# Kernel optimization log

Measured on AMD Instinct MI355X. Metric: run time of the kernel, lower is better.

The kernel has to match this reference:

```python
import jax, jax.numpy as jnp
import numpy as np

N = 100000      # nodes
E = 1600000     # edges (avg degree 16)
F_IN, F_HID, F_OUT = 128, 64, 47


def setup_inputs() -> dict:
    key = jax.random.key(0)
    k1, k2, k3, k4 = jax.random.split(key, 4)
    x = jax.random.normal(k1, (N, F_IN), jnp.float32)
    edge_index = jax.random.randint(k2, (2, E), 0, N, jnp.int32)
    W1 = jax.random.normal(k3, (F_IN, F_HID), jnp.float32) * (1.0 / np.sqrt(F_IN))
    b1 = jnp.zeros((F_HID,), jnp.float32)
    W2 = jax.random.normal(k4, (F_HID, F_OUT), jnp.float32) * (1.0 / np.sqrt(F_HID))
    b2 = jnp.zeros((F_OUT,), jnp.float32)
    return {"x": x, "edge_index": edge_index, "W1": W1, "b1": b1, "W2": W2, "b2": b2}


def _gcn_conv(x, W, b, src, dst, n):
    """GCNConv with self-loops and symmetric normalization:
       out = D^{-1/2} (A + I) D^{-1/2} X W + b
    """
    xw = x @ W                                   # [N, F_out] transform first (small GEMM)
    # degree of A + I computed over destination nodes
    deg = jnp.ones((n,), xw.dtype).at[dst].add(1.0)      # [N]
    dinv = jax.lax.rsqrt(deg)                            # deg^{-1/2}
    norm = dinv[src] * dinv[dst]                         # [E]
    msg = xw[src] * norm[:, None]                        # [E, F_out] gather
    agg = jnp.zeros_like(xw).at[dst].add(msg)            # scatter-add aggregate
    agg = agg + xw * (1.0 / deg)[:, None]                # self-loop term: norm = 1/deg
    return agg + b


def reference(x, edge_index, W1, b1, W2, b2):
    src, dst = edge_index[0], edge_index[1]
    n = x.shape[0]
    h = _gcn_conv(x, W1, b1, src, dst, n)
    h = jax.nn.relu(h)
    # dropout is identity in eval mode (deterministic baseline)
    h = _gcn_conv(h, W2, b2, src, dst, n)
    return jax.nn.log_softmax(h, axis=1)
```

## Files before the change

### kernel.cpp

```cpp
#include <hip/hip_runtime.h>
#include <hip/hip_bf16.h>
#include <math.h>


#define CAP 48
#define NBSHIFT 8
#define SCNODES 256
#define BCAP 6144
typedef unsigned short u16;

__device__ __forceinline__ u16 f2bf(float f) {
    __hip_bfloat16 h = __float2bfloat16(f);
    return *reinterpret_cast<u16*>(&h);
}
__device__ __forceinline__ float bf2f(u16 u) {
    return __uint_as_float(((unsigned)u) << 16);
}


#define KC 32
#define KCP 36
#define FUSED_SMEM 18944

__global__ __launch_bounds__(256) void gemm1_bin(const float* __restrict__ X,
                                                 const float* __restrict__ W,
                                                 u16* __restrict__ OUT,
                                                 const int* __restrict__ src,
                                                 const int* __restrict__ dst,
                                                 int* __restrict__ gtail,
                                                 int* __restrict__ bucketed,
                                                 int N, int E, int NB, int seg, int BINB) {
    __shared__ __align__(16) char smem[FUSED_SMEM];
    const int t = threadIdx.x;

    if ((int)blockIdx.x >= BINB) {
        float* xs = (float*)smem;
        float* Wp = (float*)(smem + 64 * KCP * 4);
        const int row0 = (blockIdx.x - BINB) * 64;
        const int c4 = (t & 15) * 4;
        const int r4 = (t >> 4) * 4;
        float acc[4][4] = {};

        for (int k0 = 0; k0 < 128; k0 += KC) {
            const float4* W4 = reinterpret_cast<const float4*>(W + k0 * 64);
            #pragma unroll
            for (int i = t; i < KC * 16; i += 256)
                reinterpret_cast<float4*>(Wp)[i] = W4[i];
            #pragma unroll
            for (int i = t; i < 64 * 8; i += 256) {
                int r = i >> 3, kq = i & 7;
                int m = row0 + r;
                float4 v = make_float4(0.f, 0.f, 0.f, 0.f);
                if (m < N) v = *reinterpret_cast<const float4*>(&X[(size_t)m * 128 + k0 + kq * 4]);
                *reinterpret_cast<float4*>(&xs[r * KCP + kq * 4]) = v;
            }
            __syncthreads();

            for (int k = 0; k < KC; k += 4) {
                float4 A[4], B[4];
                #pragma unroll
                for (int i = 0; i < 4; i++)
                    A[i] = *reinterpret_cast<const float4*>(&xs[(r4 + i) * KCP + k]);
                #pragma unroll
                for (int kk = 0; kk < 4; kk++)
                    B[kk] = *reinterpret_cast<const float4*>(&Wp[(k + kk) * 64 + c4]);
                const float* Af = reinterpret_cast<const float*>(A);
                const float* Bf = reinterpret_cast<const float*>(B);
                #pragma unroll
                for (int i = 0; i < 4; i++)
                    #pragma unroll
                    for (int kk = 0; kk < 4; kk++) {
                        float av = Af[i * 4 + kk];
                        #pragma unroll
                        for (int j = 0; j < 4; j++)
                            acc[i][j] = fmaf(av, Bf[kk * 4 + j], acc[i][j]);
                    }
            }
            __syncthreads();
        }
        #pragma unroll
        for (int i = 0; i < 4; i++) {
            int m = row0 + r4 + i;
            if (m >= N) continue;
            ushort4 o;
            o.x = f2bf(acc[i][0]); o.y = f2bf(acc[i][1]);
            o.z = f2bf(acc[i][2]); o.w = f2bf(acc[i][3]);
            *reinterpret_cast<ushort4*>(&OUT[(size_t)m * 64 + c4]) = o;
        }
    } else {
        int* hist  = (int*)smem;
        int* scan  = hist + 512;
        int* gbase = scan + 512;
        int* srec  = (int*)(smem + 6144);
        const int bid = blockIdx.x;

        const int b0 = bid * seg;
        const int b1 = min(b0 + seg, E);
        const int n = b1 - b0;

        hist[t] = 0; hist[t + 256] = 0;
        __syncthreads();
        for (int e = b0 + t; e < b1; e += 256)
            atomicAdd(&hist[dst[e] >> NBSHIFT], 1);
        __syncthreads();
        int c0 = hist[t], c1 = hist[t + 256];
        gbase[t]       = c0 ? atomicAdd(&gtail[t], c0) : 0;
        gbase[t + 256] = c1 ? atomicAdd(&gtail[t + 256], c1) : 0;
        scan[t] = c0; scan[t + 256] = c1;
        hist[t] = 0; hist[t + 256] = 0;
        __syncthreads();
        #pragma unroll
        for (int d = 1; d < 512; d <<= 1) {
            int v0 = (t >= d) ? scan[t - d] : 0;
            int v1 = scan[t + 256 - d];
            __syncthreads();
            scan[t] += v0; scan[t + 256] += v1;
            __syncthreads();
        }
        scan[t] -= c0; scan[t + 256] -= c1;
        __syncthreads();
        for (int e = b0 + t; e < b1; e += 256) {
            int d = dst[e];
            int b = d >> NBSHIFT;
            int off = atomicAdd(&hist[b], 1);
            srec[scan[b] + off] = (src[e] << NBSHIFT) | (d & (SCNODES - 1));
        }
        __syncthreads();
        for (int b = t; b < NB; b += 256) {
            int lb = scan[b];
            int le = (b + 1 < 512) ? scan[b + 1] : n;
            int gb = gbase[b];
            for (int i = lb; i < le; i++) {
                int gpos = gb + (i - lb);
                if (gpos < BCAP) bucketed[(size_t)b * BCAP + gpos] = srec[i];
            }
        }
    }
}


__global__ __launch_bounds__(512) void scatter_csr(const int* __restrict__ bucketed,
                                                   const int* __restrict__ gtail,
                                                   int* __restrict__ cnt,
                                                   int* __restrict__ csr_src,
                                                   float* __restrict__ dinv, int N) {
    __shared__ int cntL[SCNODES];
    __shared__ __align__(16) int csrL[SCNODES * CAP];
    const int b = blockIdx.x;
    const int t = threadIdx.x;
    for (int i = t; i < SCNODES; i += 512) cntL[i] = 0;
    __syncthreads();

    int n = gtail[b]; if (n > BCAP) n = BCAP;
    const int* p = bucketed + (size_t)b * BCAP;
    for (int i = t; i < n; i += 512) {
        int rec = p[i];
        int l = rec & (SCNODES - 1);
        int slot = atomicAdd(&cntL[l], 1);
        if (slot < CAP) csrL[l * CAP + slot] = rec >> NBSHIFT;
    }
    __syncthreads();

    const int v0 = b << NBSHIFT;
    const int lim = min(SCNODES, N - v0);
    if (lim <= 0) return;
    int4* dst4 = reinterpret_cast<int4*>(&csr_src[(size_t)v0 * CAP]);
    const int4* src4 = reinterpret_cast<const int4*>(csrL);
    for (int i = t; i < lim * (CAP / 4); i += 512) dst4[i] = src4[i];
    for (int i = t; i < lim; i += 512) {
        int cv = cntL[i];
        cnt[v0 + i] = cv;
        dinv[v0 + i] = rsqrtf((float)cv + 1.0f);
    }
}


#define G2_SMEM (64 * KCP * 4 + KC * 64 * 4)

__global__ __launch_bounds__(256) void gemm2_tiled(const u16* __restrict__ X,
                                                   const float* __restrict__ W,
                                                   u16* __restrict__ OUT, int N) {
    __shared__ __align__(16) char smem[G2_SMEM];
    float* xs = (float*)smem;
    float* Wp = (float*)(smem + 64 * KCP * 4);
    const int t = threadIdx.x;
    const int row0 = blockIdx.x * 64;
    const int c4 = (t & 15) * 4;
    const int r4 = (t >> 4) * 4;
    float acc[4][4] = {};

    for (int k0 = 0; k0 < 64; k0 += KC) {
        for (int i = t; i < KC * 64; i += 256) {
            int k = i >> 6, c = i & 63;
            Wp[i] = (c < 47) ? W[(k0 + k) * 47 + c] : 0.f;
        }
        {
            int i = t;
            int r = i >> 2, kq = i & 3;
            int m = row0 + r;
            uint4 q = make_uint4(0u, 0u, 0u, 0u);
            if (m < N) q = *reinterpret_cast<const uint4*>(&X[(size_t)m * 64 + k0 + kq * 8]);
            float f0o = bf2f(q.x & 0xffffu), f1 = bf2f(q.x >> 16);
            float f2 = bf2f(q.y & 0xffffu), f3 = bf2f(q.y >> 16);
            float f4 = bf2f(q.z & 0xffffu), f5 = bf2f(q.z >> 16);
            float f6 = bf2f(q.w & 0xffffu), f7 = bf2f(q.w >> 16);
            float* dstp = &xs[r * KCP + kq * 8];
            *reinterpret_cast<float4*>(dstp)     = make_float4(f0o, f1, f2, f3);
            *reinterpret_cast<float4*>(dstp + 4) = make_float4(f4, f5, f6, f7);
        }
        __syncthreads();

        for (int k = 0; k < KC; k += 4) {
            float4 A[4], B[4];
            #pragma unroll
            for (int i = 0; i < 4; i++)
                A[i] = *reinterpret_cast<const float4*>(&xs[(r4 + i) * KCP + k]);
            #pragma unroll
            for (int kk = 0; kk < 4; kk++)
                B[kk] = *reinterpret_cast<const float4*>(&Wp[(k + kk) * 64 + c4]);
            const float* Af = reinterpret_cast<const float*>(A);
            const float* Bf = reinterpret_cast<const float*>(B);
            #pragma unroll
            for (int i = 0; i < 4; i++)
                #pragma unroll
                for (int kk = 0; kk < 4; kk++) {
                    float av = Af[i * 4 + kk];
                    #pragma unroll
                    for (int j = 0; j < 4; j++)
                        acc[i][j] = fmaf(av, Bf[kk * 4 + j], acc[i][j]);
                }
        }
        __syncthreads();
    }
    #pragma unroll
    for (int i = 0; i < 4; i++) {
        int m = row0 + r4 + i;
        if (m >= N) continue;
        ushort4 o;
        o.x = f2bf(acc[i][0]); o.y = f2bf(acc[i][1]);
        o.z = f2bf(acc[i][2]); o.w = f2bf(acc[i][3]);
        *reinterpret_cast<ushort4*>(&OUT[(size_t)m * 64 + c4]) = o;
    }
}

__device__ __forceinline__ void fma_bf8(uint4 q, float w, float* acc) {
    acc[0] = fmaf(__uint_as_float(q.x << 16),          w, acc[0]);
    acc[1] = fmaf(__uint_as_float(q.x & 0xffff0000u),  w, acc[1]);
    acc[2] = fmaf(__uint_as_float(q.y << 16),          w, acc[2]);
    acc[3] = fmaf(__uint_as_float(q.y & 0xffff0000u),  w, acc[3]);
    acc[4] = fmaf(__uint_as_float(q.z << 16),          w, acc[4]);
    acc[5] = fmaf(__uint_as_float(q.z & 0xffff0000u),  w, acc[5]);
    acc[6] = fmaf(__uint_as_float(q.w << 16),          w, acc[6]);
    acc[7] = fmaf(__uint_as_float(q.w & 0xffff0000u),  w, acc[7]);
}

#define AGG_BLOCK(TBL, SRCV, SHIFT, UMAX)                                             \
    {                                                                                 \
        int s8[UMAX];                                                                 \
        _Pragma("unroll")                                                             \
        for (int u = 0; u < UMAX; u++)                                                \
            s8[u] = __shfl(SRCV, base + u * 4 + r);                                   \
        float d8[UMAX]; uint4 q8[UMAX];                                               \
        _Pragma("unroll")                                                             \
        for (int u = 0; u < UMAX; u++) {                                              \
            if ((SHIFT) + u * 4 < cemax) {                                            \
                d8[u] = dinv[s8[u]];                                                  \
                const u16* ap = &TBL[(size_t)s8[u] * 64 + b * 8];                     \
                asm volatile("global_load_dwordx4 %0, %1, off"                        \
                             : "=v"(q8[u]) : "v"(ap));                                \
            }                                                                         \
        }                                                                             \
        asm volatile("s_waitcnt vmcnt(0)" ::: "memory");                              \
        __builtin_amdgcn_sched_barrier(0);                                            \
        _Pragma("unroll")                                                             \
        for (int u = 0; u < UMAX; u++) {                                              \
            if ((SHIFT) + u * 4 < cemax) {                                            \
                int e = (SHIFT) + u * 4 + r;                                          \
                float w = (e <= c) ? d8[u] * dv : 0.f;                                \
                fma_bf8(q8[u], w, acc);                                               \
            }                                                                         \
        }                                                                             \
    }


__global__ __launch_bounds__(256, 4) void agg1_relu(const u16* __restrict__ xw,
                                                    const int* __restrict__ csr_src,
                                                    const int* __restrict__ cnt,
                                                    const float* __restrict__ dinv,
                                                    const float* __restrict__ bias,
                                                    u16* __restrict__ h, int N) {
    const int wid = (blockIdx.x * 256 + threadIdx.x) >> 6;
    const int lane = threadIdx.x & 63;
    const int v = wid * 2 + (lane >> 5);
    if (wid * 2 >= N) return;
    const bool okv = v < N;
    const int vs = okv ? v : 0;
    const int hl = lane & 31;
    int c = okv ? cnt[vs] : 0; if (c > CAP - 1) c = CAP - 1;
    const float dv = okv ? dinv[vs] : 0.f;
    int rawA = csr_src[vs * CAP + hl];
    int sA = (hl < c) ? rawA : ((hl == c) ? vs : 0);

    int ce = c + 1;
    int cemax = max(ce, __shfl_xor(ce, 32));
    const int r = hl >> 3, b = hl & 7;
    const int base = lane & 32;
    float acc[8] = {};

    AGG_BLOCK(xw, sA, 0, 8)
    if (cemax > 32) {
        int rawB = csr_src[vs * CAP + 32 + hl];
        int hl32 = hl + 32;
        int sB = (hl32 < c) ? rawB : ((hl32 == c) ? vs : 0);
        AGG_BLOCK(xw, sB, 32, 4)
    }

    #pragma unroll
    for (int u = 0; u < 8; u++) {
        acc[u] += __shfl_xor(acc[u], 8);
        acc[u] += __shfl_xor(acc[u], 16);
    }
    if (r == 0 && okv) {
        ushort4 oA, oB;
        oA.x = f2bf(fmaxf(acc[0] + bias[b * 8 + 0], 0.f));
        oA.y = f2bf(fmaxf(acc[1] + bias[b * 8 + 1], 0.f));
        oA.z = f2bf(fmaxf(acc[2] + bias[b * 8 + 2], 0.f));
        oA.w = f2bf(fmaxf(acc[3] + bias[b * 8 + 3], 0.f));
        oB.x = f2bf(fmaxf(acc[4] + bias[b * 8 + 4], 0.f));
        oB.y = f2bf(fmaxf(acc[5] + bias[b * 8 + 5], 0.f));
        oB.z = f2bf(fmaxf(acc[6] + bias[b * 8 + 6], 0.f));
        oB.w = f2bf(fmaxf(acc[7] + bias[b * 8 + 7], 0.f));
        u16* dstp = &h[(size_t)v * 64 + b * 8];
        *reinterpret_cast<ushort4*>(dstp)     = oA;
        *reinterpret_cast<ushort4*>(dstp + 4) = oB;
    }
}


__global__ __launch_bounds__(256, 4) void agg2_lsm(const u16* __restrict__ hw,
                                                   const int* __restrict__ csr_src,
                                                   const int* __restrict__ cnt,
                                                   const float* __restrict__ dinv,
                                                   const float* __restrict__ bias,
                                                   float* __restrict__ out, int N) {
    const int wid = (blockIdx.x * 256 + threadIdx.x) >> 6;
    const int lane = threadIdx.x & 63;
    const int v = wid * 2 + (lane >> 5);
    if (wid * 2 >= N) return;
    const bool okv = v < N;
    const int vs = okv ? v : 0;
    const int hl = lane & 31;
    int c = okv ? cnt[vs] : 0; if (c > CAP - 1) c = CAP - 1;
    const float dv = okv ? dinv[vs] : 0.f;
    int rawA = csr_src[vs * CAP + hl];
    int sA = (hl < c) ? rawA : ((hl == c) ? vs : 0);

    int ce = c + 1;
    int cemax = max(ce, __shfl_xor(ce, 32));
    const int r = hl >> 3, b = hl & 7;
    const int base = lane & 32;
    float acc[8] = {};

    AGG_BLOCK(hw, sA, 0, 8)
    if (cemax > 32) {
        int rawB = csr_src[vs * CAP + 32 + hl];
        int hl32 = hl + 32;
        int sB = (hl32 < c) ? rawB : ((hl32 == c) ? vs : 0);
        AGG_BLOCK(hw, sB, 32, 4)
    }

    #pragma unroll
    for (int u = 0; u < 8; u++) {
        acc[u] += __shfl_xor(acc[u], 8);
        acc[u] += __shfl_xor(acc[u], 16);
    }
    const int f0 = b * 8;
    float val[8];
    #pragma unroll
    for (int u = 0; u < 8; u++) {
        int f = f0 + u;
        val[u] = (f < 47) ? acc[u] + bias[f] : -INFINITY;
    }
    float m = val[0];
    #pragma unroll
    for (int u = 1; u < 8; u++) m = fmaxf(m, val[u]);
    m = fmaxf(m, __shfl_xor(m, 1));
    m = fmaxf(m, __shfl_xor(m, 2));
    m = fmaxf(m, __shfl_xor(m, 4));
    float s = 0.f;
    #pragma unroll
    for (int u = 0; u < 8; u++)
        s += (f0 + u < 47) ? __expf(val[u] - m) : 0.f;
    s += __shfl_xor(s, 1);
    s += __shfl_xor(s, 2);
    s += __shfl_xor(s, 4);
    float ls = m + __logf(s);
    if (r == 0 && okv) {
        #pragma unroll
        for (int u = 0; u < 8; u++) {
            int f = f0 + u;
            if (f < 47) out[(size_t)v * 47 + f] = val[u] - ls;
        }
    }
}


extern "C" void kernel_launch(void* const* d_in, const int* in_sizes, int n_in,
                              void* d_out, int out_size, void* d_ws, size_t ws_size,
                              hipStream_t stream) {
    const float* x  = (const float*)d_in[0];
    const int*   ei = (const int*)d_in[1];
    const float* W1 = (const float*)d_in[2];
    const float* b1 = (const float*)d_in[3];
    const float* W2 = (const float*)d_in[4];
    const float* b2 = (const float*)d_in[5];
    float* out = (float*)d_out;

    const int N = in_sizes[0] / 128;
    const int E = in_sizes[1] / 2;
    const int* src = ei;
    const int* dst = ei + E;
    const int NB = ((N - 1) >> NBSHIFT) + 1;

    char* ws = (char*)d_ws;
    size_t off = 0;
    auto alloc = [&](size_t bytes) {
        void* p = ws + off;
        off += (bytes + 255) & ~(size_t)255;
        return p;
    };
    int*   cnt      = (int*)  alloc((size_t)N * 4);
    int*   gtail    = (int*)  alloc((size_t)512 * 4);
    float* dinv     = (float*)alloc((size_t)N * 4);
    int*   csr_src  = (int*)  alloc(((size_t)N * CAP + 64) * 4);
    u16*   xw1      = (u16*)  alloc((size_t)N * 64 * 2);
    int*   bucketed = (int*)  alloc((size_t)NB * BCAP * 4);
    u16*   hbuf     = (u16*)  alloc((size_t)N * 64 * 2);
    u16*   hw2      = (u16*)  alloc((size_t)N * 64 * 2);

    hipMemsetAsync(gtail, 0, 512 * 4, stream);

    const int GB = (N + 63) / 64;
    const int BINB = 512;
    const int seg = (E + BINB - 1) / BINB;
    gemm1_bin<<<BINB + GB, 256, 0, stream>>>(x, W1, xw1, src, dst, gtail, bucketed,
                                             N, E, NB, seg, BINB);
    scatter_csr<<<NB, 512, 0, stream>>>(bucketed, gtail, cnt, csr_src, dinv, N);
    agg1_relu<<<(N + 7) / 8, 256, 0, stream>>>(xw1, csr_src, cnt, dinv, b1, hbuf, N);
    gemm2_tiled<<<(N + 63) / 64, 256, 0, stream>>>(hbuf, W2, hw2, N);
    agg2_lsm<<<(N + 7) / 8, 256, 0, stream>>>(hw2, csr_src, cnt, dinv, b2, out, N);
}
```

Baseline: 243.8 us.

## Replace LDS-tiled GEMM1 with per-wave register GEMM using broadcast X loads

The first-layer GEMM no longer stages X and W tiles in shared memory with block barriers. Each wave now handles 64 rows, eight at a time: every lane owns one output column, keeps 32 W values in registers, and reads X rows as wave-uniform broadcast loads. The aim is to drop the LDS traffic and __syncthreads, at the cost of reloading W from cache once per row group and doing more scalar global loads. Grid size shrinks to 256 rows per block.

```diff
diff --git a/kernel.cpp b/kernel.cpp
--- a/kernel.cpp
+++ b/kernel.cpp
@@ -34,58 +34,34 @@
     const int t = threadIdx.x;
 
     if ((int)blockIdx.x >= BINB) {
-        float* xs = (float*)smem;
-        float* Wp = (float*)(smem + 64 * KCP * 4);
-        const int row0 = (blockIdx.x - BINB) * 64;
-        const int c4 = (t & 15) * 4;
-        const int r4 = (t >> 4) * 4;
-        float acc[4][4] = {};
-
-        for (int k0 = 0; k0 < 128; k0 += KC) {
-            const float4* W4 = reinterpret_cast<const float4*>(W + k0 * 64);
+        const int wave = t >> 6;
+        const int lane = t & 63;
+        const int row0 = ((int)blockIdx.x - BINB) * 256 + wave * 64;
+        for (int rb = 0; rb < 8; rb++) {
+            const int mbase = row0 + rb * 8;
+            if (mbase >= N) break;
+            float acc[8] = {0.f, 0.f, 0.f, 0.f, 0.f, 0.f, 0.f, 0.f};
+            for (int k0 = 0; k0 < 128; k0 += 32) {
+                float w[32];
+                #pragma unroll
+                for (int k = 0; k < 32; k++)
+                    w[k] = W[(k0 + k) * 64 + lane];
+                #pragma unroll
+                for (int mm = 0; mm < 8; mm++) {
+                    const int m = mbase + mm;
+                    if (m < N) {
+                        const float* __restrict__ xp = X + (size_t)m * 128 + k0;
+                        #pragma unroll
+                        for (int k = 0; k < 32; k++)
+                            acc[mm] = fmaf(xp[k], w[k], acc[mm]);
+                    }
+                }
+            }
             #pragma unroll
-            for (int i = t; i < KC * 16; i += 256)
-                reinterpret_cast<float4*>(Wp)[i] = W4[i];
-            #pragma unroll
-            for (int i = t; i < 64 * 8; i += 256) {
-                int r = i >> 3, kq = i & 7;
-                int m = row0 + r;
-                float4 v = make_float4(0.f, 0.f, 0.f, 0.f);
-                if (m < N) v = *reinterpret_cast<const float4*>(&X[(size_t)m * 128 + k0 + kq * 4]);
-                *reinterpret_cast<float4*>(&xs[r * KCP + kq * 4]) = v;
+            for (int mm = 0; mm < 8; mm++) {
+                const int m = mbase + mm;
+                if (m < N) OUT[(size_t)m * 64 + lane] = f2bf(acc[mm]);
             }
-            __syncthreads();
-
-            for (int k = 0; k < KC; k += 4) {
-                float4 A[4], B[4];
-                #pragma unroll
-                for (int i = 0; i < 4; i++)
-                    A[i] = *reinterpret_cast<const float4*>(&xs[(r4 + i) * KCP + k]);
-                #pragma unroll
-                for (int kk = 0; kk < 4; kk++)
-                    B[kk] = *reinterpret_cast<const float4*>(&Wp[(k + kk) * 64 + c4]);
-                const float* Af = reinterpret_cast<const float*>(A);
-                const float* Bf = reinterpret_cast<const float*>(B);
-                #pragma unroll
-                for (int i = 0; i < 4; i++)
-                    #pragma unroll
-                    for (int kk = 0; kk < 4; kk++) {
-                        float av = Af[i * 4 + kk];
-                        #pragma unroll
-                        for (int j = 0; j < 4; j++)
-                            acc[i][j] = fmaf(av, Bf[kk * 4 + j], acc[i][j]);
-                    }
-            }
-            __syncthreads();
-        }
-        #pragma unroll
-        for (int i = 0; i < 4; i++) {
-            int m = row0 + r4 + i;
-            if (m >= N) continue;
-            ushort4 o;
-            o.x = f2bf(acc[i][0]); o.y = f2bf(acc[i][1]);
-            o.z = f2bf(acc[i][2]); o.w = f2bf(acc[i][3]);
-            *reinterpret_cast<ushort4*>(&OUT[(size_t)m * 64 + c4]) = o;
         }
     } else {
         int* hist  = (int*)smem;
@@ -440,7 +416,7 @@
 
     hipMemsetAsync(gtail, 0, 512 * 4, stream);
 
-    const int GB = (N + 63) / 64;
+    const int GB = (N + 255) / 256;
     const int BINB = 512;
     const int seg = (E + BINB - 1) / BINB;
     gemm1_bin<<<BINB + GB, 256, 0, stream>>>(x, W1, xw1, src, dst, gtail, bucketed,
```

After: 363.4 us. 1.49x slower.
